# Kernel tuning notes

Measured on AMD Instinct MI355X. Metric: run time of the kernel, lower is better.

The kernel has to match this reference:

```python
import jax, jax.numpy as jnp
import numpy as np

B, S, H, V = 16, 128, 512, 50000
N, R = 5, 2          # mem_size, read_heads
Wd = H               # memory cell width
EPS = 1e-6
XI_SIZES = [R * Wd, R, Wd, 1, Wd, Wd, R, 1, 1, 3 * R]
XI = int(np.sum(XI_SIZES))  # 2573


def oneplus(x):
    return 1.0 + jax.nn.softplus(x)


def content_weight(M, k, beta):
    # M: [B,N,Wd], k: [B,R,Wd], beta: [B,R] -> [B,R,N]
    Mn = M / (jnp.linalg.norm(M, axis=-1, keepdims=True) + EPS)
    kn = k / (jnp.linalg.norm(k, axis=-1, keepdims=True) + EPS)
    sim = jnp.einsum('brw,bnw->brn', kn, Mn)
    return jax.nn.softmax(beta[:, :, None] * sim, axis=-1)


def setup_inputs() -> dict:
    key = jax.random.key(0)
    ks = jax.random.split(key, 8)
    emb = jax.random.normal(ks[0], (V, H), jnp.float32) * 0.02
    emb = emb.at[0].set(0.0)  # PAD row
    return {
        'source': jax.random.randint(ks[1], (B, S), 0, V),
        'source_lengths': jax.random.randint(ks[2], (B,), 1, S + 1),
        'emb': emb,
        'W_ih': jax.random.normal(ks[3], (4 * H, H + R * Wd), jnp.float32) * 0.02,
        'W_hh': jax.random.normal(ks[4], (4 * H, H), jnp.float32) * 0.02,
        'b_lstm': jnp.zeros((4 * H,), jnp.float32),
        'W_int': jax.random.normal(ks[5], (H, XI), jnp.float32) * 0.02,
        'b_int': jnp.zeros((XI,), jnp.float32),
        'W_out': jax.random.normal(ks[6], (H + R * Wd, H), jnp.float32) * 0.02,
        'b_out': jnp.zeros((H,), jnp.float32),
    }


def dnc_forward(source, emb, W_ih, W_hh, b_lstm, W_int, b_int, W_out, b_out):
    x_emb = emb[source]  # [B,S,H] embedding lookup
    splits = np.cumsum(XI_SIZES)[:-1]
    eye = jnp.eye(N, dtype=jnp.float32)

    def step(carry, x_t):
        h, c, M, u, p, L, wr, ww, r = carry
        # LSTM controller: input = [embedded token; read vectors]
        xin = jnp.concatenate([x_t, r.reshape(-1, R * Wd)], axis=-1)
        gates = xin @ W_ih.T + h @ W_hh.T + b_lstm
        i_, f_, g_, o_ = jnp.split(gates, 4, axis=-1)
        c = jax.nn.sigmoid(f_) * c + jax.nn.sigmoid(i_) * jnp.tanh(g_)
        h = jax.nn.sigmoid(o_) * jnp.tanh(c)
        # interface vector
        xi = h @ W_int + b_int
        (rk, rb, wk, wb, e, v, fg, ga, gw, pi) = jnp.split(xi, splits, axis=-1)
        rk = rk.reshape(-1, R, Wd)
        rb = oneplus(rb)                       # [B,R]
        wb = oneplus(wb)                       # [B,1]
        e = jax.nn.sigmoid(e)                  # [B,Wd]
        fg = jax.nn.sigmoid(fg)                # [B,R]
        ga = jax.nn.sigmoid(ga)                # [B,1]
        gw = jax.nn.sigmoid(gw)                # [B,1]
        pi = jax.nn.softmax(pi.reshape(-1, R, 3), axis=-1)
        # usage / retention
        psi = jnp.prod(1.0 - fg[:, :, None] * wr, axis=1)        # [B,N]
        u = (u + ww - u * ww) * psi
        # allocation weighting (sort-based, irregular access)
        phi = jnp.argsort(u, axis=-1)
        u_s = jnp.take_along_axis(u, phi, axis=-1)
        excl = jnp.concatenate([jnp.ones_like(u_s[:, :1]), jnp.cumprod(u_s, axis=-1)[:, :-1]], axis=-1)
        a_s = (1.0 - u_s) * excl
        a = jnp.take_along_axis(a_s, jnp.argsort(phi, axis=-1), axis=-1)
        # write weighting
        cw = content_weight(M, wk[:, None, :], wb)[:, 0]         # [B,N]
        ww = gw * (ga * a + (1.0 - ga) * cw)
        # memory write
        M = M * (1.0 - ww[:, :, None] * e[:, None, :]) + ww[:, :, None] * v[:, None, :]
        # temporal link matrix + precedence
        L = (1.0 - ww[:, :, None] - ww[:, None, :]) * L + ww[:, :, None] * p[:, None, :]
        L = L * (1.0 - eye)
        p = (1.0 - ww.sum(-1, keepdims=True)) * p + ww
        # read weightings
        fw = jnp.einsum('bij,brj->bri', L, wr)
        bw = jnp.einsum('bji,brj->bri', L, wr)
        cr = content_weight(M, rk, rb)                           # [B,R,N]
        wr = pi[..., 0:1] * bw + pi[..., 1:2] * cr + pi[..., 2:3] * fw
        r = jnp.einsum('brn,bnw->brw', wr, M)                    # [B,R,Wd]
        out_t = jnp.concatenate([h, r.reshape(-1, R * Wd)], axis=-1) @ W_out + b_out
        return (h, c, M, u, p, L, wr, ww, r), out_t

    z = jnp.zeros
    init = (z((B, H)), z((B, H)), z((B, N, Wd)), z((B, N)), z((B, N)),
            z((B, N, N)), z((B, R, N)), z((B, N)), z((B, R, Wd)))
    (h, c, *_), outs = jax.lax.scan(step, init, jnp.swapaxes(x_emb, 0, 1))
    return jnp.swapaxes(outs, 0, 1), h, c


def reference(source, source_lengths, emb, W_ih, W_hh, b_lstm, W_int, b_int, W_out, b_out):
    outputs, h, c = dnc_forward(source, emb, W_ih, W_hh, b_lstm, W_int, b_int, W_out, b_out)
    return outputs, (h, c)
```

## Files before the change

### kernel.cpp

```cpp
#include <hip/hip_runtime.h>
#include <math.h>

#define EPSC 1e-6f
#define NBLK 128

#define OFF_H     0u
#define OFF_R     16384u
#define OFF_FLAGS 32768u
#define OFF_GO    36864u
#define STATE_END 40960u
#define OFF_XI    40960u
#define OFF_GX    90112u
#define OFF_HR    4284416u

typedef float f32x4 __attribute__((ext_vector_type(4)));

__device__ __forceinline__ float sigmf(float x) { return 1.0f / (1.0f + expf(-x)); }
__device__ __forceinline__ float oneplusf(float x) {
    return 1.0f + fmaxf(x, 0.0f) + log1pf(expf(-fabsf(x)));
}

__device__ __forceinline__ void gst(float* p, float v) {
    __hip_atomic_store((unsigned*)p, __float_as_uint(v),
                       __ATOMIC_RELAXED, __HIP_MEMORY_SCOPE_AGENT);
}

__device__ __forceinline__ void cld12(
    f32x4& d0, f32x4& d1, f32x4& d2, f32x4& d3, f32x4& d4, f32x4& d5,
    f32x4& d6, f32x4& d7, f32x4& d8, f32x4& d9, f32x4& d10, f32x4& d11,
    const float* p0, const float* p1, const float* p2, const float* p3,
    const float* p4, const float* p5, const float* p6, const float* p7,
    const float* p8, const float* p9, const float* p10, const float* p11)
{
    asm volatile(
        "global_load_dwordx4 %0, %12, off sc0 sc1\n\t"
        "global_load_dwordx4 %1, %13, off sc0 sc1\n\t"
        "global_load_dwordx4 %2, %14, off sc0 sc1\n\t"
        "global_load_dwordx4 %3, %15, off sc0 sc1\n\t"
        "global_load_dwordx4 %4, %16, off sc0 sc1\n\t"
        "global_load_dwordx4 %5, %17, off sc0 sc1\n\t"
        "global_load_dwordx4 %6, %18, off sc0 sc1\n\t"
        "global_load_dwordx4 %7, %19, off sc0 sc1\n\t"
        "global_load_dwordx4 %8, %20, off sc0 sc1\n\t"
        "global_load_dwordx4 %9, %21, off sc0 sc1\n\t"
        "global_load_dwordx4 %10, %22, off sc0 sc1\n\t"
        "global_load_dwordx4 %11, %23, off sc0 sc1\n\t"
        "s_waitcnt vmcnt(0)"
        : "=&v"(d0), "=&v"(d1), "=&v"(d2), "=&v"(d3), "=&v"(d4), "=&v"(d5),
          "=&v"(d6), "=&v"(d7), "=&v"(d8), "=&v"(d9), "=&v"(d10), "=&v"(d11)
        : "v"(p0), "v"(p1), "v"(p2), "v"(p3), "v"(p4), "v"(p5),
          "v"(p6), "v"(p7), "v"(p8), "v"(p9), "v"(p10), "v"(p11)
        : "memory");
}

__device__ __forceinline__ void cld8(
    f32x4& d0, f32x4& d1, f32x4& d2, f32x4& d3,
    f32x4& d4, f32x4& d5, f32x4& d6, f32x4& d7,
    const float* p0, const float* p1, const float* p2, const float* p3,
    const float* p4, const float* p5, const float* p6, const float* p7)
{
    asm volatile(
        "global_load_dwordx4 %0, %8, off sc0 sc1\n\t"
        "global_load_dwordx4 %1, %9, off sc0 sc1\n\t"
        "global_load_dwordx4 %2, %10, off sc0 sc1\n\t"
        "global_load_dwordx4 %3, %11, off sc0 sc1\n\t"
        "global_load_dwordx4 %4, %12, off sc0 sc1\n\t"
        "global_load_dwordx4 %5, %13, off sc0 sc1\n\t"
        "global_load_dwordx4 %6, %14, off sc0 sc1\n\t"
        "global_load_dwordx4 %7, %15, off sc0 sc1\n\t"
        "s_waitcnt vmcnt(0)"
        : "=&v"(d0), "=&v"(d1), "=&v"(d2), "=&v"(d3),
          "=&v"(d4), "=&v"(d5), "=&v"(d6), "=&v"(d7)
        : "v"(p0), "v"(p1), "v"(p2), "v"(p3),
          "v"(p4), "v"(p5), "v"(p6), "v"(p7)
        : "memory");
}

__device__ __forceinline__ void cld3(
    f32x4& d0, f32x4& d1, f32x4& d2,
    const float* p0, const float* p1, const float* p2)
{
    asm volatile(
        "global_load_dwordx4 %0, %3, off sc0 sc1\n\t"
        "global_load_dwordx4 %1, %4, off sc0 sc1\n\t"
        "global_load_dwordx4 %2, %5, off sc0 sc1\n\t"
        "s_waitcnt vmcnt(0)"
        : "=&v"(d0), "=&v"(d1), "=&v"(d2)
        : "v"(p0), "v"(p1), "v"(p2)
        : "memory");
}

__device__ __forceinline__ void gsync(unsigned* flags, unsigned* go, unsigned gen,
                                      int bi, int tid)
{
    __builtin_amdgcn_s_waitcnt(0);
    __syncthreads();
    if (tid == 0)
        __hip_atomic_store(&flags[bi * 32], gen, __ATOMIC_RELAXED, __HIP_MEMORY_SCOPE_AGENT);
    if (bi == 0) {
        if (tid < NBLK) {
            unsigned v;
            do {
                v = __hip_atomic_load(&flags[tid * 32], __ATOMIC_RELAXED, __HIP_MEMORY_SCOPE_AGENT);
                if (v < gen) __builtin_amdgcn_s_sleep(1);
            } while (v < gen);
        }
        __syncthreads();
        if (tid < NBLK)
            __hip_atomic_store(&go[tid * 32], gen, __ATOMIC_RELAXED, __HIP_MEMORY_SCOPE_AGENT);
    }
    if (tid == 0) {
        unsigned v;
        do {
            v = __hip_atomic_load(&go[bi * 32], __ATOMIC_RELAXED, __HIP_MEMORY_SCOPE_AGENT);
            if (v < gen) __builtin_amdgcn_s_sleep(1);
        } while (v < gen);
    }
    __syncthreads();
}

template <int K>
__device__ __forceinline__ void blk_reduce(float* v, float (*s_red)[20],
                                           float* outp, int tid)
{
#pragma unroll
    for (int i = 0; i < K; i++) {
        float x = v[i];
        for (int o = 32; o > 0; o >>= 1) x += __shfl_down(x, o, 64);
        if ((tid & 63) == 0) s_red[tid >> 6][i] = x;
    }
    __syncthreads();
    if (tid < K) outp[tid] = s_red[0][tid] + s_red[1][tid] + s_red[2][tid] + s_red[3][tid];
    __syncthreads();
}

__global__ __launch_bounds__(256, 1) void k_main(
    const float* __restrict__ W_ih, const float* __restrict__ W_hh,
    const float* __restrict__ W_int, const float* __restrict__ b_int,
    const float* __restrict__ gx, float* __restrict__ hbuf,
    float* __restrict__ rbuf, float* __restrict__ xib,
    float* __restrict__ hr, float* __restrict__ out,
    unsigned* __restrict__ flags, unsigned* __restrict__ go)
{
    const int tid = threadIdx.x;
    const int bi  = blockIdx.x;

    __shared__ __align__(16) float big_u[12288];
    __shared__ float s_part[1024];
    __shared__ float c_s[64];
    __shared__ __align__(16) float s_M[5][520];
    __shared__ float st_u[5], st_p[5], st_L[25], st_wr[10], st_ww[5];
    __shared__ float s_red[4][20];
    __shared__ float s_rb[2], s_wb, s_fg[2], s_ga, s_gw, s_pi[2][3];
    __shared__ float s_wrold[2][5], s_uu[5], s_a[5], s_wwn[5];
    __shared__ float s_pold[5], s_Lnew[25];
    __shared__ float s_zw[5], s_z[2][5], s_fw[2][5], s_bw[2][5];
    __shared__ float s_dotA[11], s_dotB[17], s_wrnew[2][5];

    const int cG  = tid & 15;
    const int ksl = tid >> 4;
    const int cg  = (cG >> 2) * 512 + bi * 4 + (cG & 3);

    if (tid < 64) c_s[tid] = 0.f;
    if (bi < 16) {
        for (int i = tid; i < 5 * 520; i += 256) (&s_M[0][0])[i] = 0.f;
        if (tid < 5)  { st_u[tid] = 0.f; st_p[tid] = 0.f; st_ww[tid] = 0.f; }
        if (tid < 25) st_L[tid] = 0.f;
        if (tid < 10) st_wr[tid] = 0.f;
    }
    __syncthreads();

    unsigned gen = 0;

#pragma unroll 1
    for (int t = 0; t < 128; t++) {
        const float* h_in  = hbuf + (t & 1) * 8192;
        float*       h_out = hbuf + ((t + 1) & 1) * 8192;

        float acc[16];
#pragma unroll
        for (int b = 0; b < 16; b++) acc[b] = 0.f;

#pragma unroll 1
        for (int hf = 0; hf < 2; hf++) {
            {
                const int b  = tid >> 4;
                const int sg = tid & 15;
                const float* pp[12];
#pragma unroll
                for (int i = 0; i < 12; i++) {
                    int kg = hf * 768 + sg * 4 + i * 64;
                    pp[i] = (kg < 512) ? h_in + b * 512 + kg
                                       : rbuf + b * 1024 + (kg - 512);
                }
                f32x4 d0, d1, d2, d3, d4, d5, d6, d7, d8, d9, d10, d11;
                cld12(d0, d1, d2, d3, d4, d5, d6, d7, d8, d9, d10, d11,
                      pp[0], pp[1], pp[2], pp[3], pp[4], pp[5],
                      pp[6], pp[7], pp[8], pp[9], pp[10], pp[11]);
                float* dst = &big_u[b * 768 + sg * 4];
                *(f32x4*)(dst + 0 * 64) = d0;  *(f32x4*)(dst + 1 * 64) = d1;
                *(f32x4*)(dst + 2 * 64) = d2;  *(f32x4*)(dst + 3 * 64) = d3;
                *(f32x4*)(dst + 4 * 64) = d4;  *(f32x4*)(dst + 5 * 64) = d5;
                *(f32x4*)(dst + 6 * 64) = d6;  *(f32x4*)(dst + 7 * 64) = d7;
                *(f32x4*)(dst + 8 * 64) = d8;  *(f32x4*)(dst + 9 * 64) = d9;
                *(f32x4*)(dst + 10 * 64) = d10; *(f32x4*)(dst + 11 * 64) = d11;
            }
            __syncthreads();
#pragma unroll
            for (int i = 0; i < 12; i++) {
                int lc = ksl * 4 + i * 64;
                int kg = hf * 768 + lc;
                const float* wp = (kg < 512) ? W_hh + (size_t)cg * 512 + kg
                                             : W_ih + (size_t)cg * 1536 + kg;
                f32x4 wv = *(const f32x4*)wp;
#pragma unroll
                for (int b = 0; b < 16; b++) {
                    f32x4 xv = *(const f32x4*)&big_u[b * 768 + lc];
                    acc[b] = fmaf(wv[0], xv[0], acc[b]);
                    acc[b] = fmaf(wv[1], xv[1], acc[b]);
                    acc[b] = fmaf(wv[2], xv[2], acc[b]);
                    acc[b] = fmaf(wv[3], xv[3], acc[b]);
                }
            }
            __syncthreads();
        }

#pragma unroll
        for (int b = 0; b < 16; b++) {
            float x = acc[b];
            x += __shfl_xor(x, 16, 64);
            x += __shfl_xor(x, 32, 64);
            acc[b] = x;
        }
        {
            int wv = tid >> 6;
            if ((tid & 63) < 16) {
#pragma unroll
                for (int b = 0; b < 16; b++)
                    s_part[(wv * 16 + cG) * 16 + b] = acc[b];
            }
        }
        __syncthreads();
        {
            int c = tid & 15, b = tid >> 4;
            float tot = s_part[(0 * 16 + c) * 16 + b] + s_part[(1 * 16 + c) * 16 + b]
                      + s_part[(2 * 16 + c) * 16 + b] + s_part[(3 * 16 + c) * 16 + b];
            int cgc = (c >> 2) * 512 + bi * 4 + (c & 3);
            tot += gx[((size_t)t * 16 + b) * 2048 + cgc];
            s_part[c * 16 + b] = tot;
        }
        __syncthreads();
        if (tid < 64) {
            int jl = tid & 3, b = tid >> 2;
            float gi  = s_part[(0 * 4 + jl) * 16 + b];
            float gf  = s_part[(1 * 4 + jl) * 16 + b];
            float gg  = s_part[(2 * 4 + jl) * 16 + b];
            float go_ = s_part[(3 * 4 + jl) * 16 + b];
            float cc = sigmf(gf) * c_s[jl * 16 + b] + sigmf(gi) * tanhf(gg);
            float hh = sigmf(go_) * tanhf(cc);
            c_s[jl * 16 + b] = cc;
            int j = bi * 4 + jl;
            gst(h_out + b * 512 + j, hh);
            hr[((size_t)t * 16 + b) * 1536 + j] = hh;
            if (t == 127) {
                out[1048576 + b * 512 + j] = hh;
                out[1048576 + 8192 + b * 512 + j] = cc;
            }
        }
        gen++;
        gsync(flags, go, gen, bi, tid);

        {
            {
                const int b = tid >> 4, s = tid & 15;
                const float* hp = h_out + b * 512 + s * 4;
                f32x4 d0, d1, d2, d3, d4, d5, d6, d7;
                cld8(d0, d1, d2, d3, d4, d5, d6, d7,
                     hp + 0 * 64, hp + 1 * 64, hp + 2 * 64, hp + 3 * 64,
                     hp + 4 * 64, hp + 5 * 64, hp + 6 * 64, hp + 7 * 64);
                float* dst = &big_u[b * 512 + s * 4];
                *(f32x4*)(dst + 0 * 64) = d0; *(f32x4*)(dst + 1 * 64) = d1;
                *(f32x4*)(dst + 2 * 64) = d2; *(f32x4*)(dst + 3 * 64) = d3;
                *(f32x4*)(dst + 4 * 64) = d4; *(f32x4*)(dst + 5 * 64) = d5;
                *(f32x4*)(dst + 6 * 64) = d6; *(f32x4*)(dst + 7 * 64) = d7;
            }
            __syncthreads();
            const int ql  = tid & 15;
            const int kcl = tid >> 4;
#pragma unroll 1
            for (int p = 0; p < 2; p++) {
                int q0 = p * 2048 + bi * 16;
                if (p == 1 && q0 >= 2573) break;
                int q  = q0 + ql;
                int qc = (q < 2573) ? q : 2572;
                float wxr[32];
#pragma unroll
                for (int i = 0; i < 32; i++)
                    wxr[i] = W_int[(size_t)(kcl * 32 + i) * 2573 + qc];
                float ax[16];
#pragma unroll
                for (int b = 0; b < 16; b++) ax[b] = 0.f;
#pragma unroll
                for (int b = 0; b < 16; b++) {
                    const f32x4* hp = (const f32x4*)&big_u[b * 512 + kcl * 32];
#pragma unroll
                    for (int i4 = 0; i4 < 8; i4++) {
                        f32x4 hv = hp[i4];
                        ax[b] = fmaf(wxr[i4 * 4 + 0], hv[0], ax[b]);
                        ax[b] = fmaf(wxr[i4 * 4 + 1], hv[1], ax[b]);
                        ax[b] = fmaf(wxr[i4 * 4 + 2], hv[2], ax[b]);
                        ax[b] = fmaf(wxr[i4 * 4 + 3], hv[3], ax[b]);
                    }
                }
#pragma unroll
                for (int b = 0; b < 16; b++) {
                    float x = ax[b];
                    x += __shfl_xor(x, 16, 64);
                    x += __shfl_xor(x, 32, 64);
                    ax[b] = x;
                }
                {
                    int wv = tid >> 6;
                    if ((tid & 63) < 16) {
#pragma unroll
                        for (int b = 0; b < 16; b++)
                            s_part[(wv * 16 + ql) * 16 + b] = ax[b];
                    }
                }
                __syncthreads();
                {
                    int q_l = tid >> 4, b = tid & 15;
                    int qq = q0 + q_l;
                    if (qq < 2573) {
                        float v = s_part[(0 + q_l) * 16 + b] + s_part[(16 + q_l) * 16 + b]
                                + s_part[(32 + q_l) * 16 + b] + s_part[(48 + q_l) * 16 + b]
                                + b_int[qq];
                        gst(&xib[b * 3072 + qq], v);
                    }
                }
                __syncthreads();
            }
        }
        gen++;
        gsync(flags, go, gen, bi, tid);

        if (bi < 16) {
            {
                const float* xs = xib + bi * 3072;
                f32x4 d0, d1, d2;
                cld3(d0, d1, d2,
                     xs + (tid + 0) * 4, xs + (tid + 256) * 4, xs + (tid + 512) * 4);
                *(f32x4*)&big_u[(tid + 0) * 4]   = d0;
                *(f32x4*)&big_u[(tid + 256) * 4] = d1;
                *(f32x4*)&big_u[(tid + 512) * 4] = d2;
            }
            __syncthreads();
            const float* xb = big_u;

            if (tid == 0) {
                s_wb = oneplusf(xb[1538]);
                s_ga = sigmf(xb[2565]);
                s_gw = sigmf(xb[2566]);
            }
            if (tid == 1 || tid == 2) {
                int rr = tid - 1;
                s_rb[rr] = oneplusf(xb[1024 + rr]);
                s_fg[rr] = sigmf(xb[2563 + rr]);
                float z0 = xb[2567 + rr * 3], z1 = xb[2568 + rr * 3], z2 = xb[2569 + rr * 3];
                float mx = fmaxf(z0, fmaxf(z1, z2));
                float e0 = expf(z0 - mx), e1 = expf(z1 - mx), e2 = expf(z2 - mx);
                float s = e0 + e1 + e2;
                s_pi[rr][0] = e0 / s; s_pi[rr][1] = e1 / s; s_pi[rr][2] = e2 / s;
            }
            if (tid >= 32 && tid < 42) { int i = tid - 32; s_wrold[i / 5][i % 5] = st_wr[i]; }
            if (tid >= 64 && tid < 69) { s_pold[tid - 64] = st_p[tid - 64]; }
            __syncthreads();
            if (tid < 5) {
                float psi = (1.f - s_fg[0] * s_wrold[0][tid]) * (1.f - s_fg[1] * s_wrold[1][tid]);
                float un = (st_u[tid] + st_ww[tid] - st_u[tid] * st_ww[tid]) * psi;
                s_uu[tid] = un; st_u[tid] = un;
            }
            __syncthreads();
            if (tid < 5) {
                float excl = 1.f;
#pragma unroll
                for (int m2 = 0; m2 < 5; m2++) {
                    bool before = (s_uu[m2] < s_uu[tid]) || (s_uu[m2] == s_uu[tid] && m2 < tid);
                    if (before) excl *= s_uu[m2];
                }
                s_a[tid] = (1.f - s_uu[tid]) * excl;
            }
            float accA[11];
#pragma unroll
            for (int i = 0; i < 11; i++) accA[i] = 0.f;
            for (int w = tid; w < 512; w += 256) {
                float wk = xb[1026 + w];
                accA[10] += wk * wk;
#pragma unroll
                for (int n = 0; n < 5; n++) {
                    float m_ = s_M[n][w];
                    accA[n]     += m_ * m_;
                    accA[5 + n] += wk * m_;
                }
            }
            blk_reduce<11>(accA, s_red, s_dotA, tid);
            if (tid < 5) {
                float sim = s_dotA[5 + tid] /
                            ((sqrtf(s_dotA[10]) + EPSC) * (sqrtf(s_dotA[tid]) + EPSC));
                s_zw[tid] = s_wb * sim;
            }
            __syncthreads();
            if (tid < 5) {
                float mx = s_zw[0];
#pragma unroll
                for (int m2 = 1; m2 < 5; m2++) mx = fmaxf(mx, s_zw[m2]);
                float sum = 0.f;
#pragma unroll
                for (int m2 = 0; m2 < 5; m2++) sum += expf(s_zw[m2] - mx);
                float cw = expf(s_zw[tid] - mx) / sum;
                float w_ = s_gw * (s_ga * s_a[tid] + (1.f - s_ga) * cw);
                s_wwn[tid] = w_; st_ww[tid] = w_;
            }
            __syncthreads();
            float accB[17];
#pragma unroll
            for (int i = 0; i < 17; i++) accB[i] = 0.f;
            for (int w = tid; w < 512; w += 256) {
                float ew = sigmf(xb[1539 + w]);
                float vw = xb[2051 + w];
                float rk0 = xb[w], rk1 = xb[512 + w];
                accB[15] += rk0 * rk0; accB[16] += rk1 * rk1;
#pragma unroll
                for (int n = 0; n < 5; n++) {
                    float m_ = s_M[n][w];
                    float mn_ = m_ * (1.f - s_wwn[n] * ew) + s_wwn[n] * vw;
                    s_M[n][w] = mn_;
                    accB[n]      += mn_ * mn_;
                    accB[5 + n]  += rk0 * mn_;
                    accB[10 + n] += rk1 * mn_;
                }
            }
            blk_reduce<17>(accB, s_red, s_dotB, tid);
            if (tid < 25) {
                int i2 = tid / 5, j2 = tid % 5;
                float Ln = (i2 == j2) ? 0.f
                         : (1.f - s_wwn[i2] - s_wwn[j2]) * st_L[tid] + s_wwn[i2] * s_pold[j2];
                s_Lnew[tid] = Ln; st_L[tid] = Ln;
            }
            __syncthreads();
            if (tid < 5) {
                float wsum = s_wwn[0] + s_wwn[1] + s_wwn[2] + s_wwn[3] + s_wwn[4];
                st_p[tid] = (1.f - wsum) * s_pold[tid] + s_wwn[tid];
            }
            if (tid < 10) {
                int rr = tid / 5, ii = tid % 5;
                float fw = 0.f, bw = 0.f;
#pragma unroll
                for (int j2 = 0; j2 < 5; j2++) {
                    fw += s_Lnew[ii * 5 + j2] * s_wrold[rr][j2];
                    bw += s_Lnew[j2 * 5 + ii] * s_wrold[rr][j2];
                }
                s_fw[rr][ii] = fw; s_bw[rr][ii] = bw;
                float sim = s_dotB[5 + rr * 5 + ii] /
                            ((sqrtf(s_dotB[15 + rr]) + EPSC) * (sqrtf(s_dotB[ii]) + EPSC));
                s_z[rr][ii] = s_rb[rr] * sim;
            }
            __syncthreads();
            if (tid < 10) {
                int rr = tid / 5, ii = tid % 5;
                float mx = s_z[rr][0];
#pragma unroll
                for (int m2 = 1; m2 < 5; m2++) mx = fmaxf(mx, s_z[rr][m2]);
                float sum = 0.f;
#pragma unroll
                for (int m2 = 0; m2 < 5; m2++) sum += expf(s_z[rr][m2] - mx);
                float cr = expf(s_z[rr][ii] - mx) / sum;
                float wn = s_pi[rr][0] * s_bw[rr][ii] + s_pi[rr][1] * cr + s_pi[rr][2] * s_fw[rr][ii];
                s_wrnew[rr][ii] = wn; st_wr[rr * 5 + ii] = wn;
            }
            __syncthreads();
            for (int idx = tid; idx < 1024; idx += 256) {
                int rr = idx >> 9, w = idx & 511;
                float rv = 0.f;
#pragma unroll
                for (int n = 0; n < 5; n++) rv += s_wrnew[rr][n] * s_M[n][w];
                gst(&rbuf[bi * 1024 + idx], rv);
                hr[((size_t)t * 16 + bi) * 1536 + 512 + idx] = rv;
            }
        }
        gen++;
        gsync(flags, go, gen, bi, tid);
    }
}

__global__ __launch_bounds__(256) void k_embgx(
    const int* __restrict__ src, const float* __restrict__ emb,
    const float* __restrict__ W_ih, const float* __restrict__ b_lstm,
    float* __restrict__ gx)
{
    __shared__ __align__(16) float As[16][68];
    __shared__ __align__(16) float Bs[16][68];
    const int tid = threadIdx.x;
    const int bm = blockIdx.x, bn = blockIdx.y;
    const int tm = tid >> 4, tn = tid & 15;
    float acc[4][4] = {};
    for (int k0 = 0; k0 < 512; k0 += 16) {
#pragma unroll
        for (int i = 0; i < 4; i++) {
            int idx = tid + 256 * i;
            int m = idx >> 4, kk = idx & 15;
            int tok = bm * 64 + m;
            int row = src[(tok & 15) * 128 + (tok >> 4)];
            As[kk][m] = emb[(size_t)row * 512 + k0 + kk];
        }
#pragma unroll
        for (int i = 0; i < 4; i++) {
            int idx = tid + 256 * i;
            int n = idx >> 4, kk = idx & 15;
            Bs[kk][n] = W_ih[(size_t)(bn * 64 + n) * 1536 + k0 + kk];
        }
        __syncthreads();
#pragma unroll
        for (int kk = 0; kk < 16; kk++) {
            float4 av = *(const float4*)&As[kk][tm * 4];
            float4 bv = *(const float4*)&Bs[kk][tn * 4];
            float a[4] = {av.x, av.y, av.z, av.w};
            float b[4] = {bv.x, bv.y, bv.z, bv.w};
#pragma unroll
            for (int i = 0; i < 4; i++)
#pragma unroll
                for (int j = 0; j < 4; j++) acc[i][j] = fmaf(a[i], b[j], acc[i][j]);
        }
        __syncthreads();
    }
#pragma unroll
    for (int i = 0; i < 4; i++) {
        int tok = bm * 64 + tm * 4 + i;
#pragma unroll
        for (int j = 0; j < 4; j++) {
            int col = bn * 64 + tn * 4 + j;
            gx[(size_t)tok * 2048 + col] = acc[i][j] + b_lstm[col];
        }
    }
}

__global__ __launch_bounds__(256) void k_out(
    const float* __restrict__ hr, const float* __restrict__ W_out,
    const float* __restrict__ b_out, float* __restrict__ out)
{
    __shared__ __align__(16) float As[16][68];
    __shared__ __align__(16) float Bs[16][68];
    const int tid = threadIdx.x;
    const int bm = blockIdx.x, bn = blockIdx.y;
    const int tm = tid >> 4, tn = tid & 15;
    float acc[4][4] = {};
    for (int k0 = 0; k0 < 1536; k0 += 16) {
#pragma unroll
        for (int i = 0; i < 4; i++) {
            int idx = tid + 256 * i;
            int m = idx >> 4, kk = idx & 15;
            As[kk][m] = hr[(size_t)(bm * 64 + m) * 1536 + k0 + kk];
        }
#pragma unroll
        for (int i = 0; i < 4; i++) {
            int idx = tid + 256 * i;
            int kk = idx >> 6, n = idx & 63;
            Bs[kk][n] = W_out[(size_t)(k0 + kk) * 512 + bn * 64 + n];
        }
        __syncthreads();
#pragma unroll
        for (int kk = 0; kk < 16; kk++) {
            float4 av = *(const float4*)&As[kk][tm * 4];
            float4 bv = *(const float4*)&Bs[kk][tn * 4];
            float a[4] = {av.x, av.y, av.z, av.w};
            float b[4] = {bv.x, bv.y, bv.z, bv.w};
#pragma unroll
            for (int i = 0; i < 4; i++)
#pragma unroll
                for (int j = 0; j < 4; j++) acc[i][j] = fmaf(a[i], b[j], acc[i][j]);
        }
        __syncthreads();
    }
#pragma unroll
    for (int i = 0; i < 4; i++) {
        int tok = bm * 64 + tm * 4 + i;
        int b_ = tok & 15, s_ = tok >> 4;
#pragma unroll
        for (int j = 0; j < 4; j++) {
            int qn = bn * 64 + tn * 4 + j;
            out[(size_t)((b_ << 7) + s_) * 512 + qn] = acc[i][j] + b_out[qn];
        }
    }
}

extern "C" void kernel_launch(void* const* d_in, const int* in_sizes, int n_in,
                              void* d_out, int out_size, void* d_ws, size_t ws_size,
                              hipStream_t stream)
{
    const int*   src    = (const int*)d_in[0];
    const float* emb    = (const float*)d_in[2];
    const float* W_ih   = (const float*)d_in[3];
    const float* W_hh   = (const float*)d_in[4];
    const float* b_lstm = (const float*)d_in[5];
    const float* W_int  = (const float*)d_in[6];
    const float* b_int  = (const float*)d_in[7];
    const float* W_out  = (const float*)d_in[8];
    const float* b_out  = (const float*)d_in[9];

    float* ws  = (float*)d_ws;
    float* out = (float*)d_out;

    float*    hbuf  = ws + OFF_H;
    float*    rbuf  = ws + OFF_R;
    unsigned* flags = (unsigned*)(ws + OFF_FLAGS);
    unsigned* go    = (unsigned*)(ws + OFF_GO);
    float*    xib   = ws + OFF_XI;
    float*    gx    = ws + OFF_GX;
    float*    hrb   = ws + OFF_HR;

    hipMemsetAsync(ws, 0, STATE_END * sizeof(float), stream);

    k_embgx<<<dim3(32, 32), 256, 0, stream>>>(src, emb, W_ih, b_lstm, gx);

    k_main<<<dim3(NBLK), dim3(256), 0, stream>>>(
        W_ih, W_hh, W_int, b_int, gx, hbuf, rbuf, xib, hrb, out, flags, go);

    k_out<<<dim3(32, 8), 256, 0, stream>>>(hrb, W_out, b_out, out);
}
```

Measured before the change: 4.440 ms.

## Double block size, flatten barrier to all-poll flags, restage LDS with padded layout

```diff
diff --git a/kernel.cpp b/kernel.cpp
--- a/kernel.cpp
+++ b/kernel.cpp
@@ -25,95 +25,69 @@
                        __ATOMIC_RELAXED, __HIP_MEMORY_SCOPE_AGENT);
 }
 
-__device__ __forceinline__ void cld12(
+__device__ __forceinline__ void stage12(
     f32x4& d0, f32x4& d1, f32x4& d2, f32x4& d3, f32x4& d4, f32x4& d5,
     f32x4& d6, f32x4& d7, f32x4& d8, f32x4& d9, f32x4& d10, f32x4& d11,
-    const float* p0, const float* p1, const float* p2, const float* p3,
-    const float* p4, const float* p5, const float* p6, const float* p7,
-    const float* p8, const float* p9, const float* p10, const float* p11)
+    const float* ph, const float* pr)
 {
     asm volatile(
         "global_load_dwordx4 %0, %12, off sc0 sc1\n\t"
-        "global_load_dwordx4 %1, %13, off sc0 sc1\n\t"
-        "global_load_dwordx4 %2, %14, off sc0 sc1\n\t"
-        "global_load_dwordx4 %3, %15, off sc0 sc1\n\t"
-        "global_load_dwordx4 %4, %16, off sc0 sc1\n\t"
-        "global_load_dwordx4 %5, %17, off sc0 sc1\n\t"
-        "global_load_dwordx4 %6, %18, off sc0 sc1\n\t"
-        "global_load_dwordx4 %7, %19, off sc0 sc1\n\t"
-        "global_load_dwordx4 %8, %20, off sc0 sc1\n\t"
-        "global_load_dwordx4 %9, %21, off sc0 sc1\n\t"
-        "global_load_dwordx4 %10, %22, off sc0 sc1\n\t"
-        "global_load_dwordx4 %11, %23, off sc0 sc1\n\t"
+        "global_load_dwordx4 %1, %12, off offset:512 sc0 sc1\n\t"
+        "global_load_dwordx4 %2, %12, off offset:1024 sc0 sc1\n\t"
+        "global_load_dwordx4 %3, %12, off offset:1536 sc0 sc1\n\t"
+        "global_load_dwordx4 %4, %13, off sc0 sc1\n\t"
+        "global_load_dwordx4 %5, %13, off offset:512 sc0 sc1\n\t"
+        "global_load_dwordx4 %6, %13, off offset:1024 sc0 sc1\n\t"
+        "global_load_dwordx4 %7, %13, off offset:1536 sc0 sc1\n\t"
+        "global_load_dwordx4 %8, %13, off offset:2048 sc0 sc1\n\t"
+        "global_load_dwordx4 %9, %13, off offset:2560 sc0 sc1\n\t"
+        "global_load_dwordx4 %10, %13, off offset:3072 sc0 sc1\n\t"
+        "global_load_dwordx4 %11, %13, off offset:3584 sc0 sc1\n\t"
         "s_waitcnt vmcnt(0)"
         : "=&v"(d0), "=&v"(d1), "=&v"(d2), "=&v"(d3), "=&v"(d4), "=&v"(d5),
           "=&v"(d6), "=&v"(d7), "=&v"(d8), "=&v"(d9), "=&v"(d10), "=&v"(d11)
-        : "v"(p0), "v"(p1), "v"(p2), "v"(p3), "v"(p4), "v"(p5),
-          "v"(p6), "v"(p7), "v"(p8), "v"(p9), "v"(p10), "v"(p11)
+        : "v"(ph), "v"(pr)
         : "memory");
 }
 
-__device__ __forceinline__ void cld8(
-    f32x4& d0, f32x4& d1, f32x4& d2, f32x4& d3,
-    f32x4& d4, f32x4& d5, f32x4& d6, f32x4& d7,
-    const float* p0, const float* p1, const float* p2, const float* p3,
-    const float* p4, const float* p5, const float* p6, const float* p7)
+__device__ __forceinline__ void cld4o(
+    f32x4& d0, f32x4& d1, f32x4& d2, f32x4& d3, const float* p)
 {
     asm volatile(
-        "global_load_dwordx4 %0, %8, off sc0 sc1\n\t"
-        "global_load_dwordx4 %1, %9, off sc0 sc1\n\t"
-        "global_load_dwordx4 %2, %10, off sc0 sc1\n\t"
-        "global_load_dwordx4 %3, %11, off sc0 sc1\n\t"
-        "global_load_dwordx4 %4, %12, off sc0 sc1\n\t"
-        "global_load_dwordx4 %5, %13, off sc0 sc1\n\t"
-        "global_load_dwordx4 %6, %14, off sc0 sc1\n\t"
-        "global_load_dwordx4 %7, %15, off sc0 sc1\n\t"
+        "global_load_dwordx4 %0, %4, off sc0 sc1\n\t"
+        "global_load_dwordx4 %1, %4, off offset:512 sc0 sc1\n\t"
+        "global_load_dwordx4 %2, %4, off offset:1024 sc0 sc1\n\t"
+        "global_load_dwordx4 %3, %4, off offset:1536 sc0 sc1\n\t"
         "s_waitcnt vmcnt(0)"
-        : "=&v"(d0), "=&v"(d1), "=&v"(d2), "=&v"(d3),
-          "=&v"(d4), "=&v"(d5), "=&v"(d6), "=&v"(d7)
-        : "v"(p0), "v"(p1), "v"(p2), "v"(p3),
-          "v"(p4), "v"(p5), "v"(p6), "v"(p7)
+        : "=&v"(d0), "=&v"(d1), "=&v"(d2), "=&v"(d3)
+        : "v"(p)
         : "memory");
 }
 
-__device__ __forceinline__ void cld3(
-    f32x4& d0, f32x4& d1, f32x4& d2,
-    const float* p0, const float* p1, const float* p2)
+__device__ __forceinline__ void cld2(
+    f32x4& d0, f32x4& d1, const float* p, const float* q)
 {
     asm volatile(
-        "global_load_dwordx4 %0, %3, off sc0 sc1\n\t"
-        "global_load_dwordx4 %1, %4, off sc0 sc1\n\t"
-        "global_load_dwordx4 %2, %5, off sc0 sc1\n\t"
+        "global_load_dwordx4 %0, %2, off sc0 sc1\n\t"
+        "global_load_dwordx4 %1, %3, off sc0 sc1\n\t"
         "s_waitcnt vmcnt(0)"
-        : "=&v"(d0), "=&v"(d1), "=&v"(d2)
-        : "v"(p0), "v"(p1), "v"(p2)
+        : "=&v"(d0), "=&v"(d1)
+        : "v"(p), "v"(q)
         : "memory");
 }
 
-__device__ __forceinline__ void gsync(unsigned* flags, unsigned* go, unsigned gen,
+__device__ __forceinline__ void gsync(unsigned* flags, unsigned gen,
                                       int bi, int tid)
 {
     __builtin_amdgcn_s_waitcnt(0);
     __syncthreads();
     if (tid == 0)
         __hip_atomic_store(&flags[bi * 32], gen, __ATOMIC_RELAXED, __HIP_MEMORY_SCOPE_AGENT);
-    if (bi == 0) {
-        if (tid < NBLK) {
-            unsigned v;
-            do {
-                v = __hip_atomic_load(&flags[tid * 32], __ATOMIC_RELAXED, __HIP_MEMORY_SCOPE_AGENT);
-                if (v < gen) __builtin_amdgcn_s_sleep(1);
-            } while (v < gen);
-        }
-        __syncthreads();
-        if (tid < NBLK)
-            __hip_atomic_store(&go[tid * 32], gen, __ATOMIC_RELAXED, __HIP_MEMORY_SCOPE_AGENT);
-    }
-    if (tid == 0) {
+    if (tid < NBLK) {
         unsigned v;
         do {
-            v = __hip_atomic_load(&go[bi * 32], __ATOMIC_RELAXED, __HIP_MEMORY_SCOPE_AGENT);
-            if (v < gen) __builtin_amdgcn_s_sleep(1);
+            v = __hip_atomic_load(&flags[tid * 32], __ATOMIC_RELAXED, __HIP_MEMORY_SCOPE_AGENT);
+            if (v < gen) __builtin_amdgcn_s_sleep(2);
         } while (v < gen);
     }
     __syncthreads();
@@ -130,40 +104,42 @@
         if ((tid & 63) == 0) s_red[tid >> 6][i] = x;
     }
     __syncthreads();
-    if (tid < K) outp[tid] = s_red[0][tid] + s_red[1][tid] + s_red[2][tid] + s_red[3][tid];
+    if (tid < K) {
+        float s = 0.f;
+#pragma unroll
+        for (int w = 0; w < 8; w++) s += s_red[w][tid];
+        outp[tid] = s;
+    }
     __syncthreads();
 }
 
-__global__ __launch_bounds__(256, 1) void k_main(
+__global__ __launch_bounds__(512, 1) void k_main(
     const float* __restrict__ W_ih, const float* __restrict__ W_hh,
     const float* __restrict__ W_int, const float* __restrict__ b_int,
     const float* __restrict__ gx, float* __restrict__ hbuf,
     float* __restrict__ rbuf, float* __restrict__ xib,
     float* __restrict__ hr, float* __restrict__ out,
-    unsigned* __restrict__ flags, unsigned* __restrict__ go)
+    unsigned* __restrict__ flags)
 {
     const int tid = threadIdx.x;
     const int bi  = blockIdx.x;
 
-    __shared__ __align__(16) float big_u[12288];
-    __shared__ float s_part[1024];
+    __shared__ __align__(16) float big_u[26624];
+    __shared__ float s_part[2048];
+    __shared__ float s_tot[256];
     __shared__ float c_s[64];
     __shared__ __align__(16) float s_M[5][520];
     __shared__ float st_u[5], st_p[5], st_L[25], st_wr[10], st_ww[5];
-    __shared__ float s_red[4][20];
+    __shared__ float s_red[8][20];
     __shared__ float s_rb[2], s_wb, s_fg[2], s_ga, s_gw, s_pi[2][3];
     __shared__ float s_wrold[2][5], s_uu[5], s_a[5], s_wwn[5];
     __shared__ float s_pold[5], s_Lnew[25];
     __shared__ float s_zw[5], s_z[2][5], s_fw[2][5], s_bw[2][5];
     __shared__ float s_dotA[11], s_dotB[17], s_wrnew[2][5];
 
-    const int cG  = tid & 15;
-    const int ksl = tid >> 4;
-    const int cg  = (cG >> 2) * 512 + bi * 4 + (cG & 3);
-
     if (tid < 64) c_s[tid] = 0.f;
     if (bi < 16) {
-        for (int i = tid; i < 5 * 520; i += 256) (&s_M[0][0])[i] = 0.f;
+        for (int i = tid; i < 5 * 520; i += 512) (&s_M[0][0])[i] = 0.f;
         if (tid < 5)  { st_u[tid] = 0.f; st_p[tid] = 0.f; st_ww[tid] = 0.f; }
         if (tid < 25) st_L[tid] = 0.f;
         if (tid < 10) st_wr[tid] = 0.f;
@@ -177,54 +153,49 @@
         const float* h_in  = hbuf + (t & 1) * 8192;
         float*       h_out = hbuf + ((t + 1) & 1) * 8192;
 
+        float gxv = 0.f;
+        if (tid < 256) {
+            int c = tid & 15, b = tid >> 4;
+            int cgc = (c >> 2) * 512 + bi * 4 + (c & 3);
+            gxv = gx[((size_t)t * 16 + b) * 2048 + cgc];
+        }
+
+        {
+            const int b5 = tid >> 5, sg = tid & 31;
+            const float* ph = h_in + b5 * 512 + sg * 4;
+            const float* pr = rbuf + b5 * 1024 + sg * 4;
+            f32x4 d0, d1, d2, d3, d4, d5, d6, d7, d8, d9, d10, d11;
+            stage12(d0, d1, d2, d3, d4, d5, d6, d7, d8, d9, d10, d11, ph, pr);
+#define STW(i, D) { int k = sg * 4 + (i) * 128; int cc = k / 48; \
+                    *(f32x4*)&big_u[b5 * 1664 + cc * 52 + (k - cc * 48)] = D; }
+            STW(0, d0)  STW(1, d1)  STW(2, d2)  STW(3, d3)
+            STW(4, d4)  STW(5, d5)  STW(6, d6)  STW(7, d7)
+            STW(8, d8)  STW(9, d9)  STW(10, d10) STW(11, d11)
+#undef STW
+        }
+        __syncthreads();
+
+        const int cG  = tid & 15;
+        const int ksG = tid >> 4;
+        const int cg  = (cG >> 2) * 512 + bi * 4 + (cG & 3);
         float acc[16];
 #pragma unroll
         for (int b = 0; b < 16; b++) acc[b] = 0.f;
-
-#pragma unroll 1
-        for (int hf = 0; hf < 2; hf++) {
-            {
-                const int b  = tid >> 4;
-                const int sg = tid & 15;
-                const float* pp[12];
-#pragma unroll
-                for (int i = 0; i < 12; i++) {
-                    int kg = hf * 768 + sg * 4 + i * 64;
-                    pp[i] = (kg < 512) ? h_in + b * 512 + kg
-                                       : rbuf + b * 1024 + (kg - 512);
-                }
-                f32x4 d0, d1, d2, d3, d4, d5, d6, d7, d8, d9, d10, d11;
-                cld12(d0, d1, d2, d3, d4, d5, d6, d7, d8, d9, d10, d11,
-                      pp[0], pp[1], pp[2], pp[3], pp[4], pp[5],
-                      pp[6], pp[7], pp[8], pp[9], pp[10], pp[11]);
-                float* dst = &big_u[b * 768 + sg * 4];
-                *(f32x4*)(dst + 0 * 64) = d0;  *(f32x4*)(dst + 1 * 64) = d1;
-                *(f32x4*)(dst + 2 * 64) = d2;  *(f32x4*)(dst + 3 * 64) = d3;
-                *(f32x4*)(dst + 4 * 64) = d4;  *(f32x4*)(dst + 5 * 64) = d5;
-                *(f32x4*)(dst + 6 * 64) = d6;  *(f32x4*)(dst + 7 * 64) = d7;
-                *(f32x4*)(dst + 8 * 64) = d8;  *(f32x4*)(dst + 9 * 64) = d9;
-                *(f32x4*)(dst + 10 * 64) = d10; *(f32x4*)(dst + 11 * 64) = d11;
-            }
-            __syncthreads();
-#pragma unroll
-            for (int i = 0; i < 12; i++) {
-                int lc = ksl * 4 + i * 64;
-                int kg = hf * 768 + lc;
-                const float* wp = (kg < 512) ? W_hh + (size_t)cg * 512 + kg
-                                             : W_ih + (size_t)cg * 1536 + kg;
-                f32x4 wv = *(const f32x4*)wp;
-#pragma unroll
-                for (int b = 0; b < 16; b++) {
-                    f32x4 xv = *(const f32x4*)&big_u[b * 768 + lc];
-                    acc[b] = fmaf(wv[0], xv[0], acc[b]);
-                    acc[b] = fmaf(wv[1], xv[1], acc[b]);
-                    acc[b] = fmaf(wv[2], xv[2], acc[b]);
-                    acc[b] = fmaf(wv[3], xv[3], acc[b]);
-                }
-            }
-            __syncthreads();
-        }
-
+#pragma unroll
+        for (int i = 0; i < 12; i++) {
+            int kg = ksG * 48 + i * 4;
+            const float* wp = (kg < 512) ? W_hh + (size_t)cg * 512 + kg
+                                         : W_ih + (size_t)cg * 1536 + kg;
+            f32x4 wv = *(const f32x4*)wp;
+#pragma unroll
+            for (int b = 0; b < 16; b++) {
+                f32x4 xv = *(const f32x4*)&big_u[b * 1664 + ksG * 52 + i * 4];
+                acc[b] = fmaf(wv[0], xv[0], acc[b]);
+                acc[b] = fmaf(wv[1], xv[1], acc[b]);
+                acc[b] = fmaf(wv[2], xv[2], acc[b]);
+                acc[b] = fmaf(wv[3], xv[3], acc[b]);
+            }
+        }
 #pragma unroll
         for (int b = 0; b < 16; b++) {
             float x = acc[b];
@@ -241,21 +212,20 @@
             }
         }
         __syncthreads();
-        {
+        if (tid < 256) {
             int c = tid & 15, b = tid >> 4;
-            float tot = s_part[(0 * 16 + c) * 16 + b] + s_part[(1 * 16 + c) * 16 + b]
-                      + s_part[(2 * 16 + c) * 16 + b] + s_part[(3 * 16 + c) * 16 + b];
-            int cgc = (c >> 2) * 512 + bi * 4 + (c & 3);
-            tot += gx[((size_t)t * 16 + b) * 2048 + cgc];
-            s_part[c * 16 + b] = tot;
+            float tot = gxv;
+#pragma unroll
+            for (int w = 0; w < 8; w++) tot += s_part[(w * 16 + c) * 16 + b];
+            s_tot[c * 16 + b] = tot;
         }
         __syncthreads();
         if (tid < 64) {
             int jl = tid & 3, b = tid >> 2;
-            float gi  = s_part[(0 * 4 + jl) * 16 + b];
-            float gf  = s_part[(1 * 4 + jl) * 16 + b];
-            float gg  = s_part[(2 * 4 + jl) * 16 + b];
-            float go_ = s_part[(3 * 4 + jl) * 16 + b];
+            float gi  = s_tot[(0 * 4 + jl) * 16 + b];
+            float gf  = s_tot[(1 * 4 + jl) * 16 + b];
+            float gg  = s_tot[(2 * 4 + jl) * 16 + b];
+            float go_ = s_tot[(3 * 4 + jl) * 16 + b];
             float cc = sigmf(gf) * c_s[jl * 16 + b] + sigmf(gi) * tanhf(gg);
             float hh = sigmf(go_) * tanhf(cc);
             c_s[jl * 16 + b] = cc;
@@ -268,43 +238,41 @@
             }
         }
         gen++;
-        gsync(flags, go, gen, bi, tid);
+        gsync(flags, gen, bi, tid);
 
         {
             {
-                const int b = tid >> 4, s = tid & 15;
-                const float* hp = h_out + b * 512 + s * 4;
-                f32x4 d0, d1, d2, d3, d4, d5, d6, d7;
-                cld8(d0, d1, d2, d3, d4, d5, d6, d7,
-                     hp + 0 * 64, hp + 1 * 64, hp + 2 * 64, hp + 3 * 64,
-                     hp + 4 * 64, hp + 5 * 64, hp + 6 * 64, hp + 7 * 64);
-                float* dst = &big_u[b * 512 + s * 4];
-                *(f32x4*)(dst + 0 * 64) = d0; *(f32x4*)(dst + 1 * 64) = d1;
-                *(f32x4*)(dst + 2 * 64) = d2; *(f32x4*)(dst + 3 * 64) = d3;
-                *(f32x4*)(dst + 4 * 64) = d4; *(f32x4*)(dst + 5 * 64) = d5;
-                *(f32x4*)(dst + 6 * 64) = d6; *(f32x4*)(dst + 7 * 64) = d7;
+                const int b5 = tid >> 5, s = tid & 31;
+                const float* ph = h_out + b5 * 512 + s * 4;
+                f32x4 e0, e1, e2, e3;
+                cld4o(e0, e1, e2, e3, ph);
+#define STX(j, E) { int k = s * 4 + (j) * 128; \
+                    *(f32x4*)&big_u[b5 * 576 + (k >> 5) * 36 + (k & 31)] = E; }
+                STX(0, e0) STX(1, e1) STX(2, e2) STX(3, e3)
+#undef STX
             }
             __syncthreads();
             const int ql  = tid & 15;
             const int kcl = tid >> 4;
 #pragma unroll 1
             for (int p = 0; p < 2; p++) {
-                int q0 = p * 2048 + bi * 16;
-                if (p == 1 && q0 >= 2573) break;
+                if (p == 1 && bi < 95) break;
+                int q0 = (p == 0) ? bi * 16 : 2048 + (bi - 95) * 16;
                 int q  = q0 + ql;
                 int qc = (q < 2573) ? q : 2572;
-                float wxr[32];
-#pragma unroll
-                for (int i = 0; i < 32; i++)
-                    wxr[i] = W_int[(size_t)(kcl * 32 + i) * 2573 + qc];
+                float wxr[16];
+#pragma unroll
+                for (int i = 0; i < 16; i++)
+                    wxr[i] = W_int[(size_t)(kcl * 16 + i) * 2573 + qc];
                 float ax[16];
 #pragma unroll
                 for (int b = 0; b < 16; b++) ax[b] = 0.f;
 #pragma unroll
                 for (int b = 0; b < 16; b++) {
-                    const f32x4* hp = (const f32x4*)&big_u[b * 512 + kcl * 32];
-#pragma unroll
-                    for (int i4 = 0; i4 < 8; i4++) {
+                    const f32x4* hp = (const f32x4*)
+                        &big_u[b * 576 + (kcl >> 1) * 36 + (kcl & 1) * 16];
+#pragma unroll
+                    for (int i4 = 0; i4 < 4; i4++) {
                         f32x4 hv = hp[i4];
                         ax[b] = fmaf(wxr[i4 * 4 + 0], hv[0], ax[b]);
                         ax[b] = fmaf(wxr[i4 * 4 + 1], hv[1], ax[b]);
@@ -328,13 +296,14 @@
                     }
                 }
                 __syncthreads();
-                {
+                if (tid < 256) {
                     int q_l = tid >> 4, b = tid & 15;
                     int qq = q0 + q_l;
                     if (qq < 2573) {
-                        float v = s_part[(0 + q_l) * 16 + b] + s_part[(16 + q_l) * 16 + b]
-                                + s_part[(32 + q_l) * 16 + b] + s_part[(48 + q_l) * 16 + b]
-                                + b_int[qq];
+                        float v = b_int[qq];
+#pragma unroll
+                        for (int w = 0; w < 8; w++)
+                            v += s_part[(w * 16 + q_l) * 16 + b];
                         gst(&xib[b * 3072 + qq], v);
                     }
                 }
@@ -342,17 +311,17 @@
             }
         }
         gen++;
-        gsync(flags, go, gen, bi, tid);
+        gsync(flags, gen, bi, tid);
 
         if (bi < 16) {
             {
                 const float* xs = xib + bi * 3072;
-                f32x4 d0, d1, d2;
-                cld3(d0, d1, d2,
-                     xs + (tid + 0) * 4, xs + (tid + 256) * 4, xs + (tid + 512) * 4);
-                *(f32x4*)&big_u[(tid + 0) * 4]   = d0;
-                *(f32x4*)&big_u[(tid + 256) * 4] = d1;
-                *(f32x4*)&big_u[(tid + 512) * 4] = d2;
+                if (tid < 384) {
+                    f32x4 d0, d1;
+                    cld2(d0, d1, xs + tid * 4, xs + (384 + tid) * 4);
+                    *(f32x4*)&big_u[tid * 4]         = d0;
+                    *(f32x4*)&big_u[(384 + tid) * 4] = d1;
+                }
             }
             __syncthreads();
             const float* xb = big_u;
@@ -393,7 +362,8 @@
             float accA[11];
 #pragma unroll
             for (int i = 0; i < 11; i++) accA[i] = 0.f;
-            for (int w = tid; w < 512; w += 256) {
+            {
+                int w = tid;
                 float wk = xb[1026 + w];
                 accA[10] += wk * wk;
 #pragma unroll
@@ -425,7 +395,8 @@
             float accB[17];
 #pragma unroll
             for (int i = 0; i < 17; i++) accB[i] = 0.f;
-            for (int w = tid; w < 512; w += 256) {
+            {
+                int w = tid;
                 float ew = sigmf(xb[1539 + w]);
                 float vw = xb[2051 + w];
                 float rk0 = xb[w], rk1 = xb[512 + w];
@@ -479,7 +450,7 @@
                 s_wrnew[rr][ii] = wn; st_wr[rr * 5 + ii] = wn;
             }
             __syncthreads();
-            for (int idx = tid; idx < 1024; idx += 256) {
+            for (int idx = tid; idx < 1024; idx += 512) {
                 int rr = idx >> 9, w = idx & 511;
                 float rv = 0.f;
 #pragma unroll
@@ -489,7 +460,7 @@
             }
         }
         gen++;
-        gsync(flags, go, gen, bi, tid);
+        gsync(flags, gen, bi, tid);
     }
 }
 
@@ -613,7 +584,6 @@
     float*    hbuf  = ws + OFF_H;
     float*    rbuf  = ws + OFF_R;
     unsigned* flags = (unsigned*)(ws + OFF_FLAGS);
-    unsigned* go    = (unsigned*)(ws + OFF_GO);
     float*    xib   = ws + OFF_XI;
     float*    gx    = ws + OFF_GX;
     float*    hrb   = ws + OFF_HR;
@@ -622,8 +592,8 @@
 
     k_embgx<<<dim3(32, 32), 256, 0, stream>>>(src, emb, W_ih, b_lstm, gx);
 
-    k_main<<<dim3(NBLK), dim3(256), 0, stream>>>(
-        W_ih, W_hh, W_int, b_int, gx, hbuf, rbuf, xib, hrb, out, flags, go);
+    k_main<<<dim3(NBLK), dim3(512), 0, stream>>>(
+        W_ih, W_hh, W_int, b_int, gx, hbuf, rbuf, xib, hrb, out, flags);
 
     k_out<<<dim3(32, 8), 256, 0, stream>>>(hrb, W_out, b_out, out);
 }
```

Measured after the change: 6.643 ms. 49.6% more time.
